# Kernel tuning notes

Measured on AMD Instinct MI355X. Metric: run time of the kernel, lower is better.

## Reference

```python
import jax, jax.numpy as jnp
import numpy as np

N = 1024
H = 1024
B, T = 64, 256


def setup_inputs() -> dict:
    key = jax.random.key(0)
    ks = jax.random.split(key, 12)
    inp = {
        "h_time": jax.random.normal(ks[0], (B, T, H), dtype=jnp.float32),
        "A_pearson": jax.random.uniform(ks[1], (N, N), dtype=jnp.float32),
        "E_dyn": jax.random.normal(ks[2], (N, H), dtype=jnp.float32) * 0.1,
        "alpha_raw": jnp.float32(0.5),
        "tau_raw": jnp.float32(1.0),
        # gate_gen: Linear(H, H//2) -> GELU -> Linear(H//2, N) -> Sigmoid
        "gate_W1": jax.random.normal(ks[3], (H, H // 2), dtype=jnp.float32) * (1.0 / np.sqrt(H)),
        "gate_b1": jnp.zeros((H // 2,), dtype=jnp.float32),
        "gate_W2": jax.random.normal(ks[4], (H // 2, N), dtype=jnp.float32) * (1.0 / np.sqrt(H // 2)),
        "gate_b2": jnp.zeros((N,), dtype=jnp.float32),
        "h2n_W": jax.random.normal(ks[5], (H, N), dtype=jnp.float32) * (1.0 / np.sqrt(H)),
        "h2n_b": jnp.zeros((N,), dtype=jnp.float32),
        "n2h_W": jax.random.normal(ks[6], (N, H), dtype=jnp.float32) * (1.0 / np.sqrt(N)),
        "n2h_b": jnp.zeros((H,), dtype=jnp.float32),
        "ln_w": jnp.ones((H,), dtype=jnp.float32),
        "ln_b": jnp.zeros((H,), dtype=jnp.float32),
    }
    return inp


def _layernorm(x, w, b, eps=1e-5):
    mu = x.mean(-1, keepdims=True)
    var = ((x - mu) ** 2).mean(-1, keepdims=True)
    return (x - mu) * jax.lax.rsqrt(var + eps) * w + b


def reference(h_time, A_pearson, E_dyn, alpha_raw, tau_raw,
              gate_W1, gate_b1, gate_W2, gate_b2,
              h2n_W, h2n_b, n2h_W, n2h_b, ln_w, ln_b):
    tau = jax.nn.softplus(tau_raw) + 1e-6
    alpha = jax.nn.sigmoid(alpha_raw)

    h_mean = h_time.mean(axis=(0, 1))                      # [H]
    E = E_dyn + h_mean[None, :]
    E_cur = E / jnp.maximum(jnp.linalg.norm(E, axis=-1, keepdims=True), 1e-12)  # F.normalize

    A_dyn = jax.nn.relu(E_cur @ E_cur.T)                   # [N,N]
    A_dyn = A_dyn / (A_dyn.sum(axis=-1, keepdims=True) + 1e-6)
    A_dyn = 0.5 * (A_dyn + A_dyn.T)
    A_base = alpha * A_pearson + (1.0 - alpha) * A_dyn

    h_gate = h_time.mean(axis=1)                           # [B,H]
    hid = jax.nn.gelu(h_gate @ gate_W1 + gate_b1, approximate=False)
    gamma = jax.nn.sigmoid(hid @ gate_W2 + gate_b2)        # [B,N]

    # Python loop over batch == row-scaling by mean gate
    A_mix = A_base * gamma.mean(axis=0)[:, None]           # [N,N]

    z_nodes = h_time @ h2n_W + h2n_b                       # [B,T,N]
    z_gcn = jnp.einsum('btn,mn->btm', z_nodes, A_mix)      # z_nodes @ A_mix.T
    msg_h = z_gcn @ n2h_W + n2h_b                          # [B,T,H]

    logits = (A_base @ E_cur) / tau                        # [N,H]
    node_attn = jax.nn.softmax(logits, axis=0)
    global_w = jnp.tanh(node_attn.mean(axis=0))            # [H]

    y = h_time * (1.0 + global_w) + msg_h
    return _layernorm(y, ln_w, ln_b)
```

## Files before the change

### kernel.cpp

```cpp
#include <hip/hip_runtime.h>
#include <math.h>

#define H 1024
#define Nn 1024
#define Bb 64
#define Tt 256
#define BT (Bb * Tt)

typedef unsigned short ushort_t;
typedef __attribute__((ext_vector_type(8))) short bf16x8;
typedef __attribute__((ext_vector_type(4))) float f32x4;


__device__ __forceinline__ ushort_t f2bf(float x) {
    union { float f; unsigned u; } v; v.f = x;
    unsigned r = v.u + 0x7FFFu + ((v.u >> 16) & 1u);
    return (ushort_t)(r >> 16);
}
__device__ __forceinline__ float bf2f(ushort_t h) {
    union { unsigned u; float f; } v; v.u = ((unsigned)h) << 16; return v.f;
}

__device__ __forceinline__ float block_reduce_sum_256(float v) {
    __shared__ float sbuf[4];
    __syncthreads();
    #pragma unroll
    for (int off = 32; off > 0; off >>= 1) v += __shfl_down(v, off, 64);
    int lane = threadIdx.x & 63, w = threadIdx.x >> 6;
    if (lane == 0) sbuf[w] = v;
    __syncthreads();
    if (threadIdx.x == 0) sbuf[0] = sbuf[0] + sbuf[1] + sbuf[2] + sbuf[3];
    __syncthreads();
    return sbuf[0];
}

__global__ void k_stage1(const float* __restrict__ h_time, float* __restrict__ hg_part,
                         ushort_t* __restrict__ ht_bf16, const float* __restrict__ n2h_b,
                         float* __restrict__ rowsumS, float* __restrict__ bias_h,
                         const float* __restrict__ n2h_W, const float* __restrict__ h2n_W,
                         const float* __restrict__ W1, const float* __restrict__ W2,
                         ushort_t* __restrict__ n2hWT_h, ushort_t* __restrict__ n2hWT_l,
                         ushort_t* __restrict__ h2nW_h, ushort_t* __restrict__ h2nW_l,
                         float* __restrict__ W1T, float* __restrict__ W2T) {
    __shared__ float tile[32][33];
    int id = blockIdx.x;
    if (id < 2048) {
        int b = id >> 5, r = id & 31;
        int z = r >> 2, cb = r & 3;
        int col = cb * 256 + threadIdx.x;
        if (b == 0 && z == 0) {
            rowsumS[col] = 0.f;
            bias_h[col] = n2h_b[col];
        }
        float s = 0.f;
        #pragma unroll 4
        for (int t = z * 32; t < z * 32 + 32; ++t) {
            size_t o = ((size_t)b * Tt + t) * H + col;
            float v = h_time[o];
            s += v;
            ht_bf16[o] = f2bf(v);
        }
        hg_part[(size_t)(b * 8 + z) * H + col] = s;
        return;
    }
    int tx = threadIdx.x & 31, ty = threadIdx.x >> 5;
    if (id < 3072) {
        int t = id - 2048;
        int i0 = (t >> 5) * 32, j0 = (t & 31) * 32;
        #pragma unroll
        for (int q = 0; q < 4; ++q)
            tile[ty + 8 * q][tx] = n2h_W[(size_t)(i0 + ty + 8 * q) * H + j0 + tx];
        __syncthreads();
        #pragma unroll
        for (int q = 0; q < 4; ++q) {
            float v = tile[tx][ty + 8 * q];
            size_t o = (size_t)(j0 + ty + 8 * q) * Nn + i0 + tx;
            ushort_t hh = f2bf(v);
            n2hWT_h[o] = hh;
            n2hWT_l[o] = f2bf(v - bf2f(hh));
        }
    } else if (id < 4096) {
        size_t idx = (size_t)(id - 3072) * 1024 + threadIdx.x * 4;
        float4 v = *(const float4*)&h2n_W[idx];
        float c[4] = {v.x, v.y, v.z, v.w};
        union { ushort_t u[4]; uint2 w; } ph, pl;
        #pragma unroll
        for (int q = 0; q < 4; ++q) {
            ph.u[q] = f2bf(c[q]);
            pl.u[q] = f2bf(c[q] - bf2f(ph.u[q]));
        }
        *(uint2*)&h2nW_h[idx] = ph.w;
        *(uint2*)&h2nW_l[idx] = pl.w;
    } else if (id < 4608) {
        int t = id - 4096;
        int i0 = (t >> 4) * 32, j0 = (t & 15) * 32;
        #pragma unroll
        for (int q = 0; q < 4; ++q)
            tile[ty + 8 * q][tx] = W1[(size_t)(i0 + ty + 8 * q) * 512 + j0 + tx];
        __syncthreads();
        #pragma unroll
        for (int q = 0; q < 4; ++q)
            W1T[(size_t)(j0 + ty + 8 * q) * 1024 + i0 + tx] = tile[tx][ty + 8 * q];
    } else {
        int t = id - 4608;
        int i0 = (t >> 5) * 32, j0 = (t & 31) * 32;
        #pragma unroll
        for (int q = 0; q < 4; ++q)
            tile[ty + 8 * q][tx] = W2[(size_t)(i0 + ty + 8 * q) * 1024 + j0 + tx];
        __syncthreads();
        #pragma unroll
        for (int q = 0; q < 4; ++q)
            W2T[(size_t)(j0 + ty + 8 * q) * 512 + i0 + tx] = tile[tx][ty + 8 * q];
    }
}

__global__ void k_stage2(const float* __restrict__ hg_part, float* __restrict__ h_gate,
                         float* __restrict__ h_mean) {
    int id = blockIdx.x;
    if (id < 256) {
        int b = id >> 2, cb = id & 3;
        int col = cb * 256 + threadIdx.x;
        float s = 0.f;
        #pragma unroll
        for (int z = 0; z < 8; ++z) s += hg_part[(size_t)(b * 8 + z) * H + col];
        h_gate[b * H + col] = s * (1.0f / Tt);
    } else {
        int h = (id - 256) * 256 + threadIdx.x;
        float s = 0.f;
        for (int r = 0; r < 512; ++r) s += hg_part[(size_t)r * H + h];
        h_mean[h] = s * (1.0f / (Bb * Tt));
    }
}

__global__ __launch_bounds__(256) void k_stage3(
    const float* __restrict__ E_dyn, const float* __restrict__ h_mean,
    ushort_t* __restrict__ E_b,
    const float* __restrict__ h_gate, const float* __restrict__ W1T,
    const float* __restrict__ b1, float* __restrict__ hid) {
    if (blockIdx.x < 1024) {
        int n = blockIdx.x;
        float e[4]; float ss = 0.f;
        #pragma unroll
        for (int q = 0; q < 4; ++q) {
            int h = threadIdx.x + 256 * q;
            e[q] = E_dyn[(size_t)n * H + h] + h_mean[h];
            ss += e[q] * e[q];
        }
        float tot = block_reduce_sum_256(ss);
        float scale = 1.0f / fmaxf(sqrtf(tot), 1e-12f);
        #pragma unroll
        for (int q = 0; q < 4; ++q) {
            int h = threadIdx.x + 256 * q;
            E_b[(size_t)n * H + h] = f2bf(e[q] * scale);
        }
        return;
    }
    int gid = (blockIdx.x - 1024) * 4 + (threadIdx.x >> 6);
    int lane = threadIdx.x & 63;
    int b = gid >> 9, j = gid & 511;
    const float* xr = h_gate + b * H;
    const float* wr = W1T + (size_t)j * H;
    float s = 0.f;
    #pragma unroll
    for (int it = 0; it < 4; ++it) {
        int k = it * 256 + lane * 4;
        float4 x4 = *(const float4*)&xr[k];
        float4 w4 = *(const float4*)&wr[k];
        s += x4.x * w4.x + x4.y * w4.y + x4.z * w4.z + x4.w * w4.w;
    }
    #pragma unroll
    for (int off = 32; off > 0; off >>= 1) s += __shfl_down(s, off, 64);
    if (lane == 0) {
        float a = s + b1[j];
        hid[b * 512 + j] = 0.5f * a * (1.0f + erff(a * 0.70710678118654752f));
    }
}

template <int PASSES, int EPI>
__device__ __forceinline__ void gemm64_body(
    int bx, int by,
    const ushort_t* __restrict__ Ah, const ushort_t* __restrict__ Al,
    const ushort_t* __restrict__ Bh, const ushort_t* __restrict__ Bl,
    ushort_t* __restrict__ O1, ushort_t* __restrict__ O2,
    float* __restrict__ fout, const float* __restrict__ fvec,
    int M, int N, int K) {
    constexpr int NST = (PASSES == 3) ? 4 : 2;
    constexpr int BUFSZ = NST * 64 * 64;
    __shared__ ushort_t sStage[2 * BUFSZ];
    const int tid = threadIdx.x, wave = tid >> 6, lane = tid & 63;
    const int quad = lane >> 4, l16 = lane & 15;
    const int m0 = by * 64, n0 = bx * 64;
    const int wm = (wave >> 1) * 32, wn = (wave & 1) * 32;
    const int sw = (l16 & 7) << 3;

    f32x4 acc[2][2];
    #pragma unroll
    for (int i = 0; i < 2; ++i)
        #pragma unroll
        for (int j = 0; j < 2; ++j)
            acc[i][j] = (f32x4){0.f, 0.f, 0.f, 0.f};

    auto stage = [&](int buf, int k0) {
        ushort_t* sAh = sStage + buf * BUFSZ;
        ushort_t* sBh = sAh + 64 * 64;
        ushort_t* sAl = sAh + 2 * 64 * 64;
        ushort_t* sBl = sAh + 3 * 64 * 64;
        #pragma unroll
        for (int inst = 0; inst < 2; ++inst) {
            const int cbase = (wave * 2 + inst) * 64;
            const int c = cbase + lane;
            const int row = c >> 3;
            const int q = (c & 7) ^ (row & 7);
            const size_t offA = (size_t)(m0 + row) * K + k0 + q * 8;
            const size_t offB = (size_t)(n0 + row) * K + k0 + q * 8;
            __builtin_amdgcn_global_load_lds(
                (const __attribute__((address_space(1))) unsigned int*)(Ah + offA),
                (__attribute__((address_space(3))) unsigned int*)&sAh[cbase * 8], 16, 0, 0);
            __builtin_amdgcn_global_load_lds(
                (const __attribute__((address_space(1))) unsigned int*)(Bh + offB),
                (__attribute__((address_space(3))) unsigned int*)&sBh[cbase * 8], 16, 0, 0);
            if constexpr (PASSES == 3) {
                __builtin_amdgcn_global_load_lds(
                    (const __attribute__((address_space(1))) unsigned int*)(Al + offA),
                    (__attribute__((address_space(3))) unsigned int*)&sAl[cbase * 8], 16, 0, 0);
                __builtin_amdgcn_global_load_lds(
                    (const __attribute__((address_space(1))) unsigned int*)(Bl + offB),
                    (__attribute__((address_space(3))) unsigned int*)&sBl[cbase * 8], 16, 0, 0);
            }
        }
    };

    auto compute = [&](int buf) {
        const ushort_t* sAh = sStage + buf * BUFSZ;
        const ushort_t* sBh = sAh + 64 * 64;
        const ushort_t* sAl = sAh + 2 * 64 * 64;
        const ushort_t* sBl = sAh + 3 * 64 * 64;
        #pragma unroll
        for (int half = 0; half < 2; ++half) {
            bf16x8 fah[2], fbh[2];
            bf16x8 fal[PASSES == 3 ? 2 : 1], fbl[PASSES == 3 ? 2 : 1];
            #pragma unroll
            for (int i = 0; i < 2; ++i) {
                const int ko = ((half * 4 + quad) << 3) ^ sw;
                fah[i] = *(const bf16x8*)&sAh[(wm + i * 16 + l16) * 64 + ko];
                fbh[i] = *(const bf16x8*)&sBh[(wn + i * 16 + l16) * 64 + ko];
                if constexpr (PASSES == 3) {
                    fal[i] = *(const bf16x8*)&sAl[(wm + i * 16 + l16) * 64 + ko];
                    fbl[i] = *(const bf16x8*)&sBl[(wn + i * 16 + l16) * 64 + ko];
                }
            }
            #pragma unroll
            for (int i = 0; i < 2; ++i)
                #pragma unroll
                for (int j = 0; j < 2; ++j) {
                    acc[i][j] = __builtin_amdgcn_mfma_f32_16x16x32_bf16(fah[i], fbh[j], acc[i][j], 0, 0, 0);
                    if constexpr (PASSES == 3) {
                        acc[i][j] = __builtin_amdgcn_mfma_f32_16x16x32_bf16(fah[i], fbl[j], acc[i][j], 0, 0, 0);
                        acc[i][j] = __builtin_amdgcn_mfma_f32_16x16x32_bf16(fal[i], fbh[j], acc[i][j], 0, 0, 0);
                    }
                }
        }
    };

    stage(0, 0);
    __syncthreads();
    int cur = 0;
    for (int k0 = 64; k0 < K; k0 += 64) {
        stage(cur ^ 1, k0);
        compute(cur);
        __syncthreads();
        cur ^= 1;
    }
    compute(cur);

    float fv[2];
    if constexpr (EPI == 2) {
        #pragma unroll
        for (int j = 0; j < 2; ++j) fv[j] = fvec[n0 + wn + j * 16 + l16];
    }
    #pragma unroll
    for (int i = 0; i < 2; ++i)
        #pragma unroll
        for (int r = 0; r < 4; ++r) {
            const int m = m0 + wm + i * 16 + quad * 4 + r;
            float rowacc = 0.f;
            #pragma unroll
            for (int j = 0; j < 2; ++j) {
                const size_t o = (size_t)m * N + n0 + wn + j * 16 + l16;
                float v = acc[i][j][r];
                if constexpr (EPI == 1) {
                    v = fmaxf(v, 0.f);
                    O1[o] = f2bf(v);
                    rowacc += v;
                } else if constexpr (EPI == 2) {
                    ushort_t hh = f2bf(v);
                    O1[o] = hh;
                    O2[o] = f2bf(v - bf2f(hh));
                    rowacc += v * fv[j];
                } else {
                    O1[o] = f2bf(v);
                }
            }
            if constexpr (EPI == 1 || EPI == 2) {
                rowacc += __shfl_xor(rowacc, 1);
                rowacc += __shfl_xor(rowacc, 2);
                rowacc += __shfl_xor(rowacc, 4);
                rowacc += __shfl_xor(rowacc, 8);
                if (l16 == 0) atomicAdd(&fout[m], rowacc);
            }
        }
}

__global__ __launch_bounds__(256) void k_stage4(
    const float* __restrict__ hid, const float* __restrict__ W2T,
    const float* __restrict__ b2, float* __restrict__ gmean,
    const ushort_t* __restrict__ E_b, ushort_t* __restrict__ Sb,
    float* __restrict__ rowsumS) {
    if (blockIdx.x < 256) {
        int n = blockIdx.x * 4 + (threadIdx.x >> 6);
        int lane = threadIdx.x & 63;
        const float* wr = W2T + (size_t)n * 512;
        float4 w0 = *(const float4*)&wr[lane * 4];
        float4 w1 = *(const float4*)&wr[256 + lane * 4];
        float bb = b2[n];
        float acc = 0.f;
        for (int b = 0; b < Bb; ++b) {
            const float* xr = hid + b * 512;
            float4 x0 = *(const float4*)&xr[lane * 4];
            float4 x1 = *(const float4*)&xr[256 + lane * 4];
            float s = x0.x * w0.x + x0.y * w0.y + x0.z * w0.z + x0.w * w0.w
                    + x1.x * w1.x + x1.y * w1.y + x1.z * w1.z + x1.w * w1.w;
            #pragma unroll
            for (int off = 32; off > 0; off >>= 1) s += __shfl_down(s, off, 64);
            if (lane == 0) acc += 1.0f / (1.0f + expf(-(s + bb)));
        }
        if (lane == 0) gmean[n] = acc * (1.0f / Bb);
        return;
    }
    int t = blockIdx.x - 256;
    gemm64_body<1, 1>(t & 15, t >> 4, E_b, nullptr, E_b, nullptr,
                      Sb, nullptr, rowsumS, nullptr, Nn, Nn, H);
}

__global__ void k_amixT(const ushort_t* __restrict__ Sb, const float* __restrict__ A_p,
                        const float* __restrict__ rowsumS, const float* __restrict__ gmean,
                        const float* __restrict__ alpha_raw,
                        ushort_t* __restrict__ Th, ushort_t* __restrict__ Tl) {
    __shared__ float tile[32][33];
    int i0 = blockIdx.y * 32, j0 = blockIdx.x * 32;
    int tx = threadIdx.x & 31, ty = threadIdx.x >> 5;
    float alpha = 1.0f / (1.0f + expf(-alpha_raw[0]));
    #pragma unroll
    for (int q = 0; q < 4; ++q) {
        int i = i0 + ty + 8 * q, j = j0 + tx;
        size_t idx = (size_t)i * Nn + j;
        float s = bf2f(Sb[idx]);
        float ad = 0.5f * s * (1.0f / (rowsumS[i] + 1e-6f) + 1.0f / (rowsumS[j] + 1e-6f));
        tile[ty + 8 * q][tx] = gmean[i] * fmaf(alpha, A_p[idx], (1.0f - alpha) * ad);
    }
    __syncthreads();
    #pragma unroll
    for (int q = 0; q < 4; ++q) {
        float v = tile[tx][ty + 8 * q];
        size_t o = (size_t)(j0 + ty + 8 * q) * Nn + i0 + tx;
        ushort_t hh = f2bf(v);
        Th[o] = hh;
        Tl[o] = f2bf(v - bf2f(hh));
    }
}

__global__ __launch_bounds__(256) void k_c1t(
    const ushort_t* __restrict__ Ah, const ushort_t* __restrict__ Al,
    const ushort_t* __restrict__ Bh, const ushort_t* __restrict__ Bl,
    ushort_t* __restrict__ O1, ushort_t* __restrict__ O2,
    float* __restrict__ fout, const float* __restrict__ fvec) {
    gemm64_body<3, 2>(blockIdx.x & 15, blockIdx.x >> 4, Ah, Al, Bh, Bl, O1, O2, fout, fvec,
                      Nn, Nn, Nn);
}
__global__ __launch_bounds__(256) void k_c2t(
    const ushort_t* __restrict__ Ah, const ushort_t* __restrict__ Al,
    const ushort_t* __restrict__ Bh, const ushort_t* __restrict__ Bl,
    ushort_t* __restrict__ O1) {
    gemm64_body<3, 3>(blockIdx.x & 15, blockIdx.x >> 4, Ah, Al, Bh, Bl, O1, nullptr,
                      nullptr, nullptr, Nn, Nn, Nn);
}

__global__ __launch_bounds__(512, 2) void gemm_big(
    const ushort_t* __restrict__ A, const ushort_t* __restrict__ Bt,
    float* __restrict__ fout, const float* __restrict__ fvec,
    int M, int N, int K) {
    constexpr int BUFSZ = 2 * 256 * 64;
    __shared__ ushort_t sStage[2 * BUFSZ];

    const int tid = threadIdx.x;
    const int wave = tid >> 6, lane = tid & 63;
    const int quad = lane >> 4, l16 = lane & 15;
    const int wr = wave >> 2, wc = wave & 3;
    const int m0 = (blockIdx.x >> 2) * 256;
    const int n0 = (blockIdx.x & 3) * 256;
    const int wm = wr * 128, wn = wc * 64;
    const int swz = l16 & 7;

    f32x4 acc[8][4];
    #pragma unroll
    for (int i = 0; i < 8; ++i)
        #pragma unroll
        for (int j = 0; j < 4; ++j)
            acc[i][j] = (f32x4){0.f, 0.f, 0.f, 0.f};

    auto stage = [&](int buf, int k0) {
        ushort_t* sA = sStage + buf * BUFSZ;
        ushort_t* sB = sA + 256 * 64;
        #pragma unroll
        for (int pass = 0; pass < 4; ++pass) {
            const int c = pass * 512 + tid;
            const int row = c >> 3;
            const int q = (c & 7) ^ (row & 7);
            const size_t offA = (size_t)(m0 + row) * K + k0 + q * 8;
            const size_t offB = (size_t)(n0 + row) * K + k0 + q * 8;
            __builtin_amdgcn_global_load_lds(
                (const __attribute__((address_space(1))) unsigned int*)(A + offA),
                (__attribute__((address_space(3))) unsigned int*)&sA[c * 8], 16, 0, 0);
            __builtin_amdgcn_global_load_lds(
                (const __attribute__((address_space(1))) unsigned int*)(Bt + offB),
                (__attribute__((address_space(3))) unsigned int*)&sB[c * 8], 16, 0, 0);
        }
    };

    stage(0, 0);
    int buf = 0;
    for (int t = 0; t < 16; ++t) {
        __syncthreads();
        if (t + 1 < 16) stage(buf ^ 1, (t + 1) * 64);
        const ushort_t* sA = sStage + buf * BUFSZ;
        const ushort_t* sB = sA + 256 * 64;
        #pragma unroll
        for (int s = 0; s < 2; ++s) {
            bf16x8 fb[4];
            #pragma unroll
            for (int j = 0; j < 4; ++j) {
                const int row = wn + j * 16 + l16;
                const int ch = (s * 4 + quad) ^ swz;
                fb[j] = *(const bf16x8*)&sB[row * 64 + ch * 8];
            }
            #pragma unroll
            for (int mh = 0; mh < 2; ++mh) {
                bf16x8 fa[4];
                #pragma unroll
                for (int i = 0; i < 4; ++i) {
                    const int row = wm + mh * 64 + i * 16 + l16;
                    const int ch = (s * 4 + quad) ^ swz;
                    fa[i] = *(const bf16x8*)&sA[row * 64 + ch * 8];
                }
                __builtin_amdgcn_s_barrier();
                asm volatile("s_waitcnt lgkmcnt(0)" ::: "memory");
                __builtin_amdgcn_sched_barrier(0);
                __builtin_amdgcn_s_setprio(1);
                #pragma unroll
                for (int i = 0; i < 4; ++i)
                    #pragma unroll
                    for (int j = 0; j < 4; ++j)
                        acc[mh * 4 + i][j] =
                            __builtin_amdgcn_mfma_f32_16x16x32_bf16(fa[i], fb[j], acc[mh * 4 + i][j], 0, 0, 0);
                __builtin_amdgcn_s_setprio(0);
                __builtin_amdgcn_s_barrier();
            }
        }
        buf ^= 1;
    }
    __syncthreads();

    float* Es = (float*)sStage + wave * 4096;
    const float SC = 1.0009765622f;

    #pragma unroll
    for (int pass = 0; pass < 2; ++pass) {
        #pragma unroll
        for (int ii = 0; ii < 4; ++ii) {
            const int i = pass * 4 + ii;
            #pragma unroll
            for (int j = 0; j < 4; ++j)
                #pragma unroll
                for (int r = 0; r < 4; ++r)
                    Es[ii * 1024 + (quad * 4 + r) * 64 + j * 16 + l16] = acc[i][j][r];
        }
        __syncthreads();
        #pragma unroll
        for (int ii = 0; ii < 4; ++ii) {
            #pragma unroll
            for (int it = 0; it < 4; ++it) {
                const int idx = it * 64 + lane;
                const int row = idx >> 4, f4 = idx & 15;
                const int m = m0 + wm + (pass * 4 + ii) * 16 + row;
                const int coln = n0 + wn + f4 * 4;
                float4 v = *(const float4*)&Es[ii * 1024 + row * 64 + f4 * 4];
                float4 b4 = *(const float4*)&fvec[coln];
                ushort4 h4 = *(const ushort4*)&A[(size_t)m * N + coln];
                float4 y;
                y.x = v.x + b4.x + SC * bf2f(h4.x);
                y.y = v.y + b4.y + SC * bf2f(h4.y);
                y.z = v.z + b4.z + SC * bf2f(h4.z);
                y.w = v.w + b4.w + SC * bf2f(h4.w);
                *(float4*)&fout[(size_t)m * N + coln] = y;
            }
        }
        __syncthreads();
    }
}

__global__ __launch_bounds__(256) void k_final_ln(const float* __restrict__ ln_w,
                                                  const float* __restrict__ ln_b,
                                                  float* __restrict__ out) {
    int wave = threadIdx.x >> 6, lane = threadIdx.x & 63;
    size_t row = (size_t)blockIdx.x * 4 + wave;
    float4 v[4];
    float s = 0.f;
    #pragma unroll
    for (int q = 0; q < 4; ++q) {
        v[q] = *(const float4*)&out[row * H + q * 256 + lane * 4];
        s += v[q].x + v[q].y + v[q].z + v[q].w;
    }
    #pragma unroll
    for (int off = 1; off < 64; off <<= 1) s += __shfl_xor(s, off, 64);
    float mu = s * (1.0f / H);
    float ss = 0.f;
    #pragma unroll
    for (int q = 0; q < 4; ++q) {
        v[q].x -= mu; v[q].y -= mu; v[q].z -= mu; v[q].w -= mu;
        ss += v[q].x * v[q].x + v[q].y * v[q].y + v[q].z * v[q].z + v[q].w * v[q].w;
    }
    #pragma unroll
    for (int off = 1; off < 64; off <<= 1) ss += __shfl_xor(ss, off, 64);
    float rstd = rsqrtf(ss * (1.0f / H) + 1e-5f);
    #pragma unroll
    for (int q = 0; q < 4; ++q) {
        int k = q * 256 + lane * 4;
        float4 w4 = *(const float4*)&ln_w[k];
        float4 b4 = *(const float4*)&ln_b[k];
        float4 o;
        o.x = fmaf(v[q].x * rstd, w4.x, b4.x);
        o.y = fmaf(v[q].y * rstd, w4.y, b4.y);
        o.z = fmaf(v[q].z * rstd, w4.z, b4.z);
        o.w = fmaf(v[q].w * rstd, w4.w, b4.w);
        *(float4*)&out[row * H + k] = o;
    }
}


extern "C" void kernel_launch(void* const* d_in, const int* in_sizes, int n_in,
                              void* d_out, int out_size, void* d_ws, size_t ws_size,
                              hipStream_t stream) {
    const float* h_time    = (const float*)d_in[0];
    const float* A_p       = (const float*)d_in[1];
    const float* E_dyn     = (const float*)d_in[2];
    const float* alpha_raw = (const float*)d_in[3];
    const float* gW1   = (const float*)d_in[5];
    const float* gb1   = (const float*)d_in[6];
    const float* gW2   = (const float*)d_in[7];
    const float* gb2   = (const float*)d_in[8];
    const float* h2n_W = (const float*)d_in[9];
    const float* h2n_b = (const float*)d_in[10];
    const float* n2h_W = (const float*)d_in[11];
    const float* n2h_b = (const float*)d_in[12];
    const float* ln_w  = (const float*)d_in[13];
    const float* ln_b  = (const float*)d_in[14];
    float* out = (float*)d_out;

    float* ws = (float*)d_ws;
    float* h_gate  = ws;  ws += Bb * H;
    float* h_mean  = ws;  ws += H;
    float* rowsumS = ws;  ws += Nn;
    float* bias_h  = ws;  ws += H;
    float* hid     = ws;  ws += Bb * 512;
    float* gmean   = ws;  ws += Nn;
    float* W1T     = ws;  ws += 512 * H;
    float* W2T     = ws;  ws += H * 512;
    float* hg_part = ws;  ws += 512 * H;
    ws += 256;
    ushort_t* E_b     = (ushort_t*)ws;  ws += (Nn * H) / 2;
    ushort_t* Sb      = (ushort_t*)ws;  ws += (Nn * Nn) / 2;
    ushort_t* AmixT_h = (ushort_t*)ws;  ws += (Nn * Nn) / 2;
    ushort_t* AmixT_l = (ushort_t*)ws;  ws += (Nn * Nn) / 2;
    ushort_t* n2hWT_h = (ushort_t*)ws;  ws += (Nn * H) / 2;
    ushort_t* n2hWT_l = (ushort_t*)ws;  ws += (Nn * H) / 2;
    ushort_t* h2nW_h  = (ushort_t*)ws;  ws += (H * Nn) / 2;
    ushort_t* h2nW_l  = (ushort_t*)ws;  ws += (H * Nn) / 2;
    ushort_t* C1Th    = (ushort_t*)ws;  ws += (H * Nn) / 2;
    ushort_t* C1Tl    = (ushort_t*)ws;  ws += (H * Nn) / 2;
    ushort_t* C2t     = (ushort_t*)ws;  ws += (H * H) / 2;
    ushort_t* ht      = (ushort_t*)ws;  ws += ((size_t)BT * H) / 2;

    k_stage1<<<5120, 256, 0, stream>>>(h_time, hg_part, ht, n2h_b, rowsumS, bias_h,
                                       n2h_W, h2n_W, gW1, gW2,
                                       n2hWT_h, n2hWT_l, h2nW_h, h2nW_l, W1T, W2T);
    k_stage2<<<260, 256, 0, stream>>>(hg_part, h_gate, h_mean);
    k_stage3<<<9216, 256, 0, stream>>>(E_dyn, h_mean, E_b, h_gate, W1T, gb1, hid);
    k_stage4<<<512, 256, 0, stream>>>(hid, W2T, gb2, gmean, E_b, Sb, rowsumS);
    k_amixT<<<dim3(32, 32), 256, 0, stream>>>(Sb, A_p, rowsumS, gmean, alpha_raw, AmixT_h, AmixT_l);
    k_c1t<<<256, 256, 0, stream>>>(n2hWT_h, n2hWT_l, AmixT_h, AmixT_l, C1Th, C1Tl, bias_h, h2n_b);
    k_c2t<<<256, 256, 0, stream>>>(C1Th, C1Tl, h2nW_h, h2nW_l, C2t);
    gemm_big<<<256, 512, 0, stream>>>(ht, C2t, out, bias_h, BT, H, H);
    k_final_ln<<<4096, 256, 0, stream>>>(ln_w, ln_b, out);
}
```

Measured before the change: 318.8 us.

## Vectorize stage1 h_time pass, remap GEMM blocks per XCD, split prefetch across k-substeps

The h_time reduction and bf16 conversion in stage1 now use float4 loads and ushort4 stores, with one block per (batch, t-chunk) covering all columns, so the grid shrinks. In gemm_big, blocks are remapped so each XCD handles a contiguous group of M tiles, which should improve L2 reuse of the A rows. The main loop now issues the next tile's prefetch in two halves interleaved with the two k-substeps. It also loads all 8 A fragments at once and does one barrier pair per substep instead of two, trading higher register pressure for fewer syncs.

```diff
diff --git a/kernel.cpp b/kernel.cpp
--- a/kernel.cpp
+++ b/kernel.cpp
@@ -44,28 +44,32 @@
                          float* __restrict__ W1T, float* __restrict__ W2T) {
     __shared__ float tile[32][33];
     int id = blockIdx.x;
-    if (id < 2048) {
-        int b = id >> 5, r = id & 31;
-        int z = r >> 2, cb = r & 3;
-        int col = cb * 256 + threadIdx.x;
+    if (id < 512) {
+        int b = id >> 3, z = id & 7;
+        int col = threadIdx.x * 4;
         if (b == 0 && z == 0) {
-            rowsumS[col] = 0.f;
-            bias_h[col] = n2h_b[col];
-        }
-        float s = 0.f;
+            #pragma unroll
+            for (int q = 0; q < 4; ++q) {
+                rowsumS[col + q] = 0.f;
+                bias_h[col + q] = n2h_b[col + q];
+            }
+        }
+        float4 s4 = {0.f, 0.f, 0.f, 0.f};
         #pragma unroll 4
         for (int t = z * 32; t < z * 32 + 32; ++t) {
             size_t o = ((size_t)b * Tt + t) * H + col;
-            float v = h_time[o];
-            s += v;
-            ht_bf16[o] = f2bf(v);
-        }
-        hg_part[(size_t)(b * 8 + z) * H + col] = s;
+            float4 v = *(const float4*)&h_time[o];
+            s4.x += v.x; s4.y += v.y; s4.z += v.z; s4.w += v.w;
+            ushort4 h;
+            h.x = f2bf(v.x); h.y = f2bf(v.y); h.z = f2bf(v.z); h.w = f2bf(v.w);
+            *(ushort4*)&ht_bf16[o] = h;
+        }
+        *(float4*)&hg_part[(size_t)(b * 8 + z) * H + col] = s4;
         return;
     }
     int tx = threadIdx.x & 31, ty = threadIdx.x >> 5;
-    if (id < 3072) {
-        int t = id - 2048;
+    if (id < 1536) {
+        int t = id - 512;
         int i0 = (t >> 5) * 32, j0 = (t & 31) * 32;
         #pragma unroll
         for (int q = 0; q < 4; ++q)
@@ -79,8 +83,8 @@
             n2hWT_h[o] = hh;
             n2hWT_l[o] = f2bf(v - bf2f(hh));
         }
-    } else if (id < 4096) {
-        size_t idx = (size_t)(id - 3072) * 1024 + threadIdx.x * 4;
+    } else if (id < 2560) {
+        size_t idx = (size_t)(id - 1536) * 1024 + threadIdx.x * 4;
         float4 v = *(const float4*)&h2n_W[idx];
         float c[4] = {v.x, v.y, v.z, v.w};
         union { ushort_t u[4]; uint2 w; } ph, pl;
@@ -91,8 +95,8 @@
         }
         *(uint2*)&h2nW_h[idx] = ph.w;
         *(uint2*)&h2nW_l[idx] = pl.w;
-    } else if (id < 4608) {
-        int t = id - 4096;
+    } else if (id < 3072) {
+        int t = id - 2560;
         int i0 = (t >> 4) * 32, j0 = (t & 15) * 32;
         #pragma unroll
         for (int q = 0; q < 4; ++q)
@@ -102,7 +106,7 @@
         for (int q = 0; q < 4; ++q)
             W1T[(size_t)(j0 + ty + 8 * q) * 1024 + i0 + tx] = tile[tx][ty + 8 * q];
     } else {
-        int t = id - 4608;
+        int t = id - 3072;
         int i0 = (t >> 5) * 32, j0 = (t & 31) * 32;
         #pragma unroll
         for (int q = 0; q < 4; ++q)
@@ -396,8 +400,9 @@
     const int wave = tid >> 6, lane = tid & 63;
     const int quad = lane >> 4, l16 = lane & 15;
     const int wr = wave >> 2, wc = wave & 3;
-    const int m0 = (blockIdx.x >> 2) * 256;
-    const int n0 = (blockIdx.x & 3) * 256;
+    const int xcd = blockIdx.x & 7, idx = blockIdx.x >> 3;
+    const int m0 = (xcd * 8 + (idx >> 2)) * 256;
+    const int n0 = (idx & 3) * 256;
     const int wm = wr * 128, wn = wc * 64;
     const int swz = l16 & 7;
 
@@ -408,12 +413,12 @@
         for (int j = 0; j < 4; ++j)
             acc[i][j] = (f32x4){0.f, 0.f, 0.f, 0.f};
 
-    auto stage = [&](int buf, int k0) {
+    auto stage_half = [&](int buf, int k0, int half) {
         ushort_t* sA = sStage + buf * BUFSZ;
         ushort_t* sB = sA + 256 * 64;
         #pragma unroll
-        for (int pass = 0; pass < 4; ++pass) {
-            const int c = pass * 512 + tid;
+        for (int pass = 0; pass < 2; ++pass) {
+            const int c = (half * 2 + pass) * 512 + tid;
             const int row = c >> 3;
             const int q = (c & 7) ^ (row & 7);
             const size_t offA = (size_t)(m0 + row) * K + k0 + q * 8;
@@ -427,44 +432,35 @@
         }
     };
 
-    stage(0, 0);
+    stage_half(0, 0, 0);
+    stage_half(0, 0, 1);
     int buf = 0;
     for (int t = 0; t < 16; ++t) {
         __syncthreads();
-        if (t + 1 < 16) stage(buf ^ 1, (t + 1) * 64);
         const ushort_t* sA = sStage + buf * BUFSZ;
         const ushort_t* sB = sA + 256 * 64;
         #pragma unroll
         for (int s = 0; s < 2; ++s) {
-            bf16x8 fb[4];
-            #pragma unroll
-            for (int j = 0; j < 4; ++j) {
-                const int row = wn + j * 16 + l16;
-                const int ch = (s * 4 + quad) ^ swz;
-                fb[j] = *(const bf16x8*)&sB[row * 64 + ch * 8];
-            }
-            #pragma unroll
-            for (int mh = 0; mh < 2; ++mh) {
-                bf16x8 fa[4];
+            if (t + 1 < 16) stage_half(buf ^ 1, (t + 1) * 64, s);
+            bf16x8 fb[4], fa[8];
+            const int ch = (s * 4 + quad) ^ swz;
+            #pragma unroll
+            for (int j = 0; j < 4; ++j)
+                fb[j] = *(const bf16x8*)&sB[(wn + j * 16 + l16) * 64 + ch * 8];
+            #pragma unroll
+            for (int i = 0; i < 8; ++i)
+                fa[i] = *(const bf16x8*)&sA[(wm + i * 16 + l16) * 64 + ch * 8];
+            __builtin_amdgcn_s_barrier();
+            asm volatile("s_waitcnt lgkmcnt(0)" ::: "memory");
+            __builtin_amdgcn_sched_barrier(0);
+            __builtin_amdgcn_s_setprio(1);
+            #pragma unroll
+            for (int i = 0; i < 8; ++i)
                 #pragma unroll
-                for (int i = 0; i < 4; ++i) {
-                    const int row = wm + mh * 64 + i * 16 + l16;
-                    const int ch = (s * 4 + quad) ^ swz;
-                    fa[i] = *(const bf16x8*)&sA[row * 64 + ch * 8];
-                }
-                __builtin_amdgcn_s_barrier();
-                asm volatile("s_waitcnt lgkmcnt(0)" ::: "memory");
-                __builtin_amdgcn_sched_barrier(0);
-                __builtin_amdgcn_s_setprio(1);
-                #pragma unroll
-                for (int i = 0; i < 4; ++i)
-                    #pragma unroll
-                    for (int j = 0; j < 4; ++j)
-                        acc[mh * 4 + i][j] =
-                            __builtin_amdgcn_mfma_f32_16x16x32_bf16(fa[i], fb[j], acc[mh * 4 + i][j], 0, 0, 0);
-                __builtin_amdgcn_s_setprio(0);
-                __builtin_amdgcn_s_barrier();
-            }
+                for (int j = 0; j < 4; ++j)
+                    acc[i][j] = __builtin_amdgcn_mfma_f32_16x16x32_bf16(fa[i], fb[j], acc[i][j], 0, 0, 0);
+            __builtin_amdgcn_s_setprio(0);
+            __builtin_amdgcn_s_barrier();
         }
         buf ^= 1;
     }
@@ -489,8 +485,8 @@
         for (int ii = 0; ii < 4; ++ii) {
             #pragma unroll
             for (int it = 0; it < 4; ++it) {
-                const int idx = it * 64 + lane;
-                const int row = idx >> 4, f4 = idx & 15;
+                const int idx2 = it * 64 + lane;
+                const int row = idx2 >> 4, f4 = idx2 & 15;
                 const int m = m0 + wm + (pass * 4 + ii) * 16 + row;
                 const int coln = n0 + wn + f4 * 4;
                 float4 v = *(const float4*)&Es[ii * 1024 + row * 64 + f4 * 4];
@@ -590,7 +586,7 @@
     ushort_t* C2t     = (ushort_t*)ws;  ws += (H * H) / 2;
     ushort_t* ht      = (ushort_t*)ws;  ws += ((size_t)BT * H) / 2;
 
-    k_stage1<<<5120, 256, 0, stream>>>(h_time, hg_part, ht, n2h_b, rowsumS, bias_h,
+    k_stage1<<<3584, 256, 0, stream>>>(h_time, hg_part, ht, n2h_b, rowsumS, bias_h,
                                        n2h_W, h2n_W, gW1, gW2,
                                        n2hWT_h, n2hWT_l, h2nW_h, h2nW_l, W1T, W2T);
     k_stage2<<<260, 256, 0, stream>>>(hg_part, h_gate, h_mean);
```

After: 316.4 us. Within noise of the previous version (-0.8%).
